# Kernel tuning notes

Hardware: AMD Instinct MI355X
Metric: run time of the kernel (lower is better)

The kernel has to match this reference:

```python
import jax, jax.numpy as jnp
import numpy as np

WIN = 8          # window_size
DIM = 96         # embedding dim
HEADS = 3        # num_heads
N = WIN * WIN    # tokens per window
B_ = 8192        # total windows (2 images * 64*64 windows)
NUM_WIN = 4096   # windows per image (mask leading dim)


def _relative_position_index():
    # Same construction as the torch module (meshgrid default 'ij').
    ch = np.arange(WIN)
    coords = np.stack(np.meshgrid(ch, ch, indexing="ij"))          # [2, W, W]
    flat = coords.reshape(2, -1)                                     # [2, N]
    rel = flat[:, :, None] - flat[:, None, :]                        # [2, N, N]
    rel = rel.transpose(1, 2, 0).astype(np.int32)                    # [N, N, 2]
    rel[:, :, 0] += WIN - 1
    rel[:, :, 1] += WIN - 1
    rel[:, :, 0] *= 2 * WIN - 1
    return rel.sum(-1)                                               # [N, N] int32


def setup_inputs() -> dict:
    key = jax.random.key(0)
    ks = jax.random.split(key, 8)
    x = jax.random.normal(ks[0], (B_, N, DIM), dtype=jnp.float32)
    mask = jax.random.normal(ks[1], (NUM_WIN, N, N), dtype=jnp.float32)
    s = 0.02
    qkv_w = jax.random.normal(ks[2], (3 * DIM, DIM), dtype=jnp.float32) * s
    qkv_b = jax.random.normal(ks[3], (3 * DIM,), dtype=jnp.float32) * s
    proj_w = jax.random.normal(ks[4], (DIM, DIM), dtype=jnp.float32) * s
    proj_b = jax.random.normal(ks[5], (DIM,), dtype=jnp.float32) * s
    n_bias = (2 * WIN - 1) * (2 * WIN - 1)  # 225
    bias_table = jax.random.normal(ks[6], (n_bias, HEADS), dtype=jnp.float32) * s
    rel_idx = jnp.asarray(_relative_position_index())  # [N, N] int32
    return {"x": x, "mask": mask, "qkv_w": qkv_w, "qkv_b": qkv_b,
            "proj_w": proj_w, "proj_b": proj_b, "bias_table": bias_table,
            "rel_idx": rel_idx}


def reference(x, mask, qkv_w, qkv_b, proj_w, proj_b, bias_table, rel_idx):
    Bw, n, C = x.shape
    hd = C // HEADS
    scale = hd ** (-0.5)
    qkv = (x @ qkv_w.T + qkv_b).reshape(Bw, n, 3, HEADS, hd)
    qkv = jnp.transpose(qkv, (2, 0, 3, 1, 4))
    q, k, v = qkv[0], qkv[1], qkv[2]
    attn = jnp.einsum("bhqd,bhkd->bhqk", q * scale, k)              # [Bw, H, n, n]
    # relative position bias gather: [n, n, H] -> [H, n, n]
    bias = bias_table[rel_idx.reshape(-1)].reshape(n, n, HEADS)
    attn = attn + jnp.transpose(bias, (2, 0, 1))[None]
    # shift mask: broadcast over (batch, heads)
    nw = mask.shape[0]
    attn = attn.reshape(Bw // nw, nw, HEADS, n, n) + mask[None, :, None]
    attn = attn.reshape(Bw, HEADS, n, n)
    attn = jax.nn.softmax(attn, axis=-1)
    out = jnp.einsum("bhqk,bhkd->bhqd", attn, v)                    # [Bw, H, n, hd]
    out = jnp.transpose(out, (0, 2, 1, 3)).reshape(Bw, n, C)
    return out @ proj_w.T + proj_b
```

## Files before the change

### kernel.cpp

```cpp
#include <hip/hip_runtime.h>

typedef __attribute__((ext_vector_type(8))) short short8v;
typedef __attribute__((ext_vector_type(4))) float f32x4;

#define INVLN2 1.4426950408889634f

__device__ __forceinline__ ushort f2bf(float f) {
  union { float f; unsigned int u; } c; c.f = f;
  return (ushort)((c.u + 0x7FFFu + ((c.u >> 16) & 1u)) >> 16);
}

__device__ __forceinline__ unsigned cvtpk(float a, float b) {
  unsigned r;
  asm("v_cvt_pk_bf16_f32 %0, %1, %2" : "=v"(r) : "v"(a), "v"(b));
  return r;
}

__device__ __forceinline__ float exp2w(float x) {
#if __has_builtin(__builtin_amdgcn_exp2f)
  return __builtin_amdgcn_exp2f(x);
#else
  return __expf(x * 0.6931471805599453f);
#endif
}

__device__ __forceinline__ short8v bits8(unsigned a, unsigned b, unsigned c, unsigned d) {
  union { unsigned u[4]; short8v s; } cv;
  cv.u[0] = a; cv.u[1] = b; cv.u[2] = c; cv.u[3] = d;
  return cv.s;
}

__global__ __launch_bounds__(256) void setup_k(
    const float* __restrict__ qkv_w, const float* __restrict__ proj_w,
    const float* __restrict__ bias_table, const int* __restrict__ rel_idx,
    const float* __restrict__ qkv_b,
    ushort* __restrict__ qkv_wb, ushort* __restrict__ proj_wb,
    float* __restrict__ bias_comb, float* __restrict__ qkv_bs) {
  const float qs = 0.17677669529663687f * INVLN2;
  int idx = blockIdx.x * 256 + threadIdx.x;
  if (idx < 27648) {
    qkv_wb[idx] = f2bf(qkv_w[idx] * (idx < 9216 ? qs : 1.0f));
  } else if (idx < 36864) {
    int i = idx - 27648;
    proj_wb[i] = f2bf(proj_w[i]);
  } else if (idx < 49152) {
    int i = idx - 36864;
    int h = i / 4096, rc = i % 4096;
    bias_comb[i] = bias_table[rel_idx[rc] * 3 + h] * INVLN2;
  } else if (idx < 49440) {
    int i = idx - 49152;
    qkv_bs[i] = qkv_b[i] * (i < 96 ? qs : 1.0f);
  }
}

__global__ __launch_bounds__(256, 2) void winattn(
    const float* __restrict__ x, const float* __restrict__ mask,
    const ushort* __restrict__ qkv_wb, const ushort* __restrict__ proj_wb,
    const float* __restrict__ bias_comb, const float* __restrict__ qkv_bs,
    const float* __restrict__ proj_b, float* __restrict__ out) {
  __shared__ ushort klds[2][64][104];
  __shared__ ushort vts[2][96][64];

  const int bb = blockIdx.x;
  const int t = threadIdx.x;
  const int w = t >> 6;
  const int lane = t & 63;
  const int l15 = lane & 15;
  const int g = lane >> 4;
  const int qrow = w * 16 + l15;

  const bool ghi = (g >= 2);
  const int srcA = l15 + 16 * ((g & 1) * 2);
  const int srcB = srcA + 16;

  float4 xr4[2][3][2];
  #pragma unroll
  for (int u = 0; u < 2; ++u) {
    const float* xr = x + ((size_t)(bb + u * 4096) * 64 + qrow) * 96 + g * 8;
    #pragma unroll
    for (int ks3 = 0; ks3 < 3; ++ks3) {
      xr4[u][ks3][0] = *reinterpret_cast<const float4*>(xr + ks3 * 32);
      xr4[u][ks3][1] = *reinterpret_cast<const float4*>(xr + ks3 * 32 + 4);
    }
  }
  const float* mrow = mask + (size_t)bb * 4096 + qrow * 64;
  float4 mk4[4];
  #pragma unroll
  for (int tj = 0; tj < 4; ++tj)
    mk4[tj] = *reinterpret_cast<const float4*>(mrow + tj * 16 + g * 4);

  short8v xa[2][3];
  #pragma unroll
  for (int u = 0; u < 2; ++u)
    #pragma unroll
    for (int ks3 = 0; ks3 < 3; ++ks3) {
      const float4 a0 = xr4[u][ks3][0], a1 = xr4[u][ks3][1];
      xa[u][ks3] = bits8(cvtpk(a0.x, a0.y), cvtpk(a0.z, a0.w),
                         cvtpk(a1.x, a1.y), cvtpk(a1.z, a1.w));
    }

  unsigned qpk[2][6][2];
  short8v bfA[3];
  float4 qbA = {0.f, 0.f, 0.f, 0.f}, qbB;
  float vbA = 0.f, vbB;
  {
    const ushort* wr = qkv_wb + l15 * 96 + g * 8;
    bfA[0] = *reinterpret_cast<const short8v*>(wr);
    bfA[1] = *reinterpret_cast<const short8v*>(wr + 32);
    bfA[2] = *reinterpret_cast<const short8v*>(wr + 64);
    qbA = *reinterpret_cast<const float4*>(qkv_bs + g * 4);
  }
  #pragma unroll
  for (int nt = 0; nt < 18; ++nt) {
    short8v bfB[3];
    if (nt < 17) {
      const ushort* wr = qkv_wb + ((nt + 1) * 16 + l15) * 96 + g * 8;
      bfB[0] = *reinterpret_cast<const short8v*>(wr);
      bfB[1] = *reinterpret_cast<const short8v*>(wr + 32);
      bfB[2] = *reinterpret_cast<const short8v*>(wr + 64);
      if (nt + 1 < 12) qbB = *reinterpret_cast<const float4*>(qkv_bs + (nt + 1) * 16 + g * 4);
      else             vbB = qkv_bs[(nt + 1) * 16 + l15];
    }
    if (nt < 6) {
      #pragma unroll
      for (int u = 0; u < 2; ++u) {
        f32x4 acc = {0.f, 0.f, 0.f, 0.f};
        #pragma unroll
        for (int ks3 = 0; ks3 < 3; ++ks3)
          acc = __builtin_amdgcn_mfma_f32_16x16x32_bf16(bfA[ks3], xa[u][ks3], acc, 0, 0, 0);
        qpk[u][nt][0] = cvtpk(acc[0] + qbA.x, acc[1] + qbA.y);
        qpk[u][nt][1] = cvtpk(acc[2] + qbA.z, acc[3] + qbA.w);
      }
    } else if (nt < 12) {
      #pragma unroll
      for (int u = 0; u < 2; ++u) {
        f32x4 acc = {0.f, 0.f, 0.f, 0.f};
        #pragma unroll
        for (int ks3 = 0; ks3 < 3; ++ks3)
          acc = __builtin_amdgcn_mfma_f32_16x16x32_bf16(bfA[ks3], xa[u][ks3], acc, 0, 0, 0);
        uint2 pk = make_uint2(cvtpk(acc[0] + qbA.x, acc[1] + qbA.y),
                              cvtpk(acc[2] + qbA.z, acc[3] + qbA.w));
        *reinterpret_cast<uint2*>(&klds[u][qrow][(nt - 6) * 16 + g * 4]) = pk;
      }
    } else {
      const int vc = nt * 16 + l15 - 192;
      const int tk = (w * 16 + g * 4) ^ ((vc & 7) << 3);
      #pragma unroll
      for (int u = 0; u < 2; ++u) {
        f32x4 acc = {0.f, 0.f, 0.f, 0.f};
        #pragma unroll
        for (int ks3 = 0; ks3 < 3; ++ks3)
          acc = __builtin_amdgcn_mfma_f32_16x16x32_bf16(xa[u][ks3], bfA[ks3], acc, 0, 0, 0);
        uint2 pk = make_uint2(cvtpk(acc[0] + vbA, acc[1] + vbA),
                              cvtpk(acc[2] + vbA, acc[3] + vbA));
        *reinterpret_cast<uint2*>(&vts[u][vc][tk]) = pk;
      }
    }
    if (nt < 17) {
      bfA[0] = bfB[0]; bfA[1] = bfB[1]; bfA[2] = bfB[2];
      qbA = qbB; vbA = vbB;
    }
  }

  short8v qf[2][3];
  #pragma unroll
  for (int u = 0; u < 2; ++u)
    #pragma unroll
    for (int h = 0; h < 3; ++h) {
      unsigned dm[4];
      #pragma unroll
      for (int m = 0; m < 4; ++m) {
        const int sl = (m < 2) ? srcA : srcB;
        unsigned lo = __shfl(qpk[u][2 * h + 0][m & 1], sl);
        unsigned hi = __shfl(qpk[u][2 * h + 1][m & 1], sl);
        dm[m] = ghi ? hi : lo;
      }
      qf[u][h] = bits8(dm[0], dm[1], dm[2], dm[3]);
    }

  const float* bcb0 = bias_comb + qrow * 64;
  float4 bc4[3][4];
  #pragma unroll
  for (int h = 0; h < 3; ++h)
    #pragma unroll
    for (int tj = 0; tj < 4; ++tj)
      bc4[h][tj] = *reinterpret_cast<const float4*>(bcb0 + h * 4096 + tj * 16 + g * 4);
  float bmk[3][4][4];
  #pragma unroll
  for (int h = 0; h < 3; ++h)
    #pragma unroll
    for (int tj = 0; tj < 4; ++tj) {
      bmk[h][tj][0] = bc4[h][tj].x + mk4[tj].x * INVLN2;
      bmk[h][tj][1] = bc4[h][tj].y + mk4[tj].y * INVLN2;
      bmk[h][tj][2] = bc4[h][tj].z + mk4[tj].z * INVLN2;
      bmk[h][tj][3] = bc4[h][tj].w + mk4[tj].w * INVLN2;
    }

  __syncthreads();

  short8v ofv[3][2];

  #pragma unroll
  for (int h = 0; h < 3; ++h) {
    f32x4 s[2][4];
    #pragma unroll
    for (int tj = 0; tj < 4; ++tj) {
      #pragma unroll
      for (int u = 0; u < 2; ++u) {
        short8v kf = *reinterpret_cast<const short8v*>(&klds[u][tj * 16 + l15][h * 32 + g * 8]);
        f32x4 z = {0.f, 0.f, 0.f, 0.f};
        s[u][tj] = __builtin_amdgcn_mfma_f32_16x16x32_bf16(kf, qf[u][h], z, 0, 0, 0);
      }
    }
    #pragma unroll
    for (int tj = 0; tj < 4; ++tj)
      #pragma unroll
      for (int u = 0; u < 2; ++u)
        #pragma unroll
        for (int r = 0; r < 4; ++r) s[u][tj][r] += bmk[h][tj][r];
    float inv[2];
    #pragma unroll
    for (int u = 0; u < 2; ++u) {
      #pragma unroll
      for (int tj = 0; tj < 4; ++tj)
        #pragma unroll
        for (int r = 0; r < 4; ++r) s[u][tj][r] = exp2w(s[u][tj][r]);
      float sm = ((s[u][0][0] + s[u][0][1]) + (s[u][0][2] + s[u][0][3]))
               + ((s[u][1][0] + s[u][1][1]) + (s[u][1][2] + s[u][1][3]))
               + ((s[u][2][0] + s[u][2][1]) + (s[u][2][2] + s[u][2][3]))
               + ((s[u][3][0] + s[u][3][1]) + (s[u][3][2] + s[u][3][3]));
      sm += __shfl_xor(sm, 16);
      sm += __shfl_xor(sm, 32);
      inv[u] = __builtin_amdgcn_rcpf(sm);
    }
    unsigned ppk[2][4][2];
    #pragma unroll
    for (int u = 0; u < 2; ++u)
      #pragma unroll
      for (int tj = 0; tj < 4; ++tj) {
        ppk[u][tj][0] = cvtpk(s[u][tj][0], s[u][tj][1]);
        ppk[u][tj][1] = cvtpk(s[u][tj][2], s[u][tj][3]);
      }
    short8v pfv[2][2];
    #pragma unroll
    for (int u = 0; u < 2; ++u)
      #pragma unroll
      for (int ks2 = 0; ks2 < 2; ++ks2) {
        unsigned dm[4];
        #pragma unroll
        for (int m = 0; m < 4; ++m) {
          const int sl = (m < 2) ? srcA : srcB;
          unsigned lo = __shfl(ppk[u][ks2 * 2 + 0][m & 1], sl);
          unsigned hi = __shfl(ppk[u][ks2 * 2 + 1][m & 1], sl);
          dm[m] = ghi ? hi : lo;
        }
        pfv[u][ks2] = bits8(dm[0], dm[1], dm[2], dm[3]);
      }
    f32x4 oacc[2][2];
    #pragma unroll
    for (int u = 0; u < 2; ++u)
      #pragma unroll
      for (int nt = 0; nt < 2; ++nt) {
        const int vc = h * 32 + nt * 16 + l15;
        f32x4 o = {0.f, 0.f, 0.f, 0.f};
        #pragma unroll
        for (int ks2 = 0; ks2 < 2; ++ks2) {
          const int tk = (ks2 * 32 + g * 8) ^ ((vc & 7) << 3);
          short8v vf = *reinterpret_cast<const short8v*>(&vts[u][vc][tk]);
          o = __builtin_amdgcn_mfma_f32_16x16x32_bf16(vf, pfv[u][ks2], o, 0, 0, 0);
        }
        oacc[u][nt] = o;
      }
    #pragma unroll
    for (int u = 0; u < 2; ++u) {
      unsigned opk[2][2];
      #pragma unroll
      for (int nt = 0; nt < 2; ++nt) {
        opk[nt][0] = cvtpk(oacc[u][nt][0] * inv[u], oacc[u][nt][1] * inv[u]);
        opk[nt][1] = cvtpk(oacc[u][nt][2] * inv[u], oacc[u][nt][3] * inv[u]);
      }
      unsigned dm[4];
      #pragma unroll
      for (int m = 0; m < 4; ++m) {
        const int sl = (m < 2) ? srcA : srcB;
        unsigned lo = __shfl(opk[0][m & 1], sl);
        unsigned hi = __shfl(opk[1][m & 1], sl);
        dm[m] = ghi ? hi : lo;
      }
      ofv[h][u] = bits8(dm[0], dm[1], dm[2], dm[3]);
    }
  }

  f32x4 pacc[2][6];
  #pragma unroll
  for (int u = 0; u < 2; ++u)
    #pragma unroll
    for (int nt2 = 0; nt2 < 6; ++nt2) pacc[u][nt2] = (f32x4){0.f, 0.f, 0.f, 0.f};
  #pragma unroll
  for (int h = 0; h < 3; ++h) {
    #pragma unroll
    for (int nt2 = 0; nt2 < 6; ++nt2) {
      short8v pfw = *reinterpret_cast<const short8v*>(proj_wb + (nt2 * 16 + l15) * 96 + h * 32 + g * 8);
      #pragma unroll
      for (int u = 0; u < 2; ++u)
        pacc[u][nt2] = __builtin_amdgcn_mfma_f32_16x16x32_bf16(ofv[h][u], pfw, pacc[u][nt2], 0, 0, 0);
    }
  }

  float pb[6];
  #pragma unroll
  for (int nt2 = 0; nt2 < 6; ++nt2) pb[nt2] = proj_b[nt2 * 16 + l15];
  #pragma unroll
  for (int u = 0; u < 2; ++u) {
    float* ob = out + (size_t)(bb + u * 4096) * 6144 + (w * 16 + g * 4) * 96 + l15;
    #pragma unroll
    for (int nt2 = 0; nt2 < 6; ++nt2)
      #pragma unroll
      for (int r = 0; r < 4; ++r)
        ob[r * 96 + nt2 * 16] = pacc[u][nt2][r] + pb[nt2];
  }
}

extern "C" void kernel_launch(void* const* d_in, const int* in_sizes, int n_in,
                              void* d_out, int out_size, void* d_ws, size_t ws_size,
                              hipStream_t stream) {
  const float* x          = (const float*)d_in[0];
  const float* mask       = (const float*)d_in[1];
  const float* qkv_w      = (const float*)d_in[2];
  const float* qkv_b      = (const float*)d_in[3];
  const float* proj_w     = (const float*)d_in[4];
  const float* proj_b     = (const float*)d_in[5];
  const float* bias_table = (const float*)d_in[6];
  const int*   rel_idx    = (const int*)d_in[7];

  char* ws = (char*)d_ws;
  ushort* qkv_wb    = (ushort*)ws;
  ushort* proj_wb   = (ushort*)(ws + 55296);
  float*  bias_comb = (float*)(ws + 55296 + 18432);
  float*  qkv_bs    = (float*)(ws + 55296 + 18432 + 49152);

  setup_k<<<194, 256, 0, stream>>>(qkv_w, proj_w, bias_table, rel_idx, qkv_b,
                                   qkv_wb, proj_wb, bias_comb, qkv_bs);
  winattn<<<4096, 256, 0, stream>>>(x, mask, qkv_wb, proj_wb,
                                    bias_comb, qkv_bs, proj_b, (float*)d_out);
}
```

Measured before the change: 167.5 us.

## Permute K, V^T and proj weight layouts to eliminate register shuffles between MFMAs

The reduction dimension of the K LDS tile, the V-transpose tile and the projection weights is permuted so that MFMA accumulator outputs can feed the next MFMA's operand directly. This removes the cross-lane __shfl sequences that previously rebuilt the Q, P and O fragments. The reduction order is the same permutation on both operands, so results stay mathematically equivalent, but correctness depends on the index maps matching exactly.

```diff
diff --git a/kernel.cpp b/kernel.cpp
--- a/kernel.cpp
+++ b/kernel.cpp
@@ -42,7 +42,11 @@
     qkv_wb[idx] = f2bf(qkv_w[idx] * (idx < 9216 ? qs : 1.0f));
   } else if (idx < 36864) {
     int i = idx - 27648;
-    proj_wb[i] = f2bf(proj_w[i]);
+    int cw = i / 96, j = i % 96;
+    int h = j >> 5, kk = j & 31;
+    int g = kk >> 3, b = (kk & 4) >> 2, d = kk & 3;
+    int src = h * 32 + 16 * b + 4 * g + d;
+    proj_wb[i] = f2bf(proj_w[cw * 96 + src]);
   } else if (idx < 49152) {
     int i = idx - 36864;
     int h = i / 4096, rc = i % 4096;
@@ -68,10 +72,6 @@
   const int l15 = lane & 15;
   const int g = lane >> 4;
   const int qrow = w * 16 + l15;
-
-  const bool ghi = (g >= 2);
-  const int srcA = l15 + 16 * ((g & 1) * 2);
-  const int srcB = srcA + 16;
 
   float4 xr4[2][3][2];
   #pragma unroll
@@ -132,6 +132,8 @@
         qpk[u][nt][1] = cvtpk(acc[2] + qbA.z, acc[3] + qbA.w);
       }
     } else if (nt < 12) {
+      const int m = nt - 6;
+      const int kcol = 32 * (m >> 1) + 8 * g + 4 * (m & 1);
       #pragma unroll
       for (int u = 0; u < 2; ++u) {
         f32x4 acc = {0.f, 0.f, 0.f, 0.f};
@@ -140,11 +142,11 @@
           acc = __builtin_amdgcn_mfma_f32_16x16x32_bf16(bfA[ks3], xa[u][ks3], acc, 0, 0, 0);
         uint2 pk = make_uint2(cvtpk(acc[0] + qbA.x, acc[1] + qbA.y),
                               cvtpk(acc[2] + qbA.z, acc[3] + qbA.w));
-        *reinterpret_cast<uint2*>(&klds[u][qrow][(nt - 6) * 16 + g * 4]) = pk;
+        *reinterpret_cast<uint2*>(&klds[u][qrow][kcol]) = pk;
       }
     } else {
       const int vc = nt * 16 + l15 - 192;
-      const int tk = (w * 16 + g * 4) ^ ((vc & 7) << 3);
+      const int tk = (32 * (w >> 1) + 8 * g + 4 * (w & 1)) ^ ((vc & 7) << 3);
       #pragma unroll
       for (int u = 0; u < 2; ++u) {
         f32x4 acc = {0.f, 0.f, 0.f, 0.f};
@@ -166,17 +168,9 @@
   #pragma unroll
   for (int u = 0; u < 2; ++u)
     #pragma unroll
-    for (int h = 0; h < 3; ++h) {
-      unsigned dm[4];
-      #pragma unroll
-      for (int m = 0; m < 4; ++m) {
-        const int sl = (m < 2) ? srcA : srcB;
-        unsigned lo = __shfl(qpk[u][2 * h + 0][m & 1], sl);
-        unsigned hi = __shfl(qpk[u][2 * h + 1][m & 1], sl);
-        dm[m] = ghi ? hi : lo;
-      }
-      qf[u][h] = bits8(dm[0], dm[1], dm[2], dm[3]);
-    }
+    for (int h = 0; h < 3; ++h)
+      qf[u][h] = bits8(qpk[u][2 * h][0], qpk[u][2 * h][1],
+                       qpk[u][2 * h + 1][0], qpk[u][2 * h + 1][1]);
 
   const float* bcb0 = bias_comb + qrow * 64;
   float4 bc4[3][4];
@@ -245,17 +239,9 @@
     #pragma unroll
     for (int u = 0; u < 2; ++u)
       #pragma unroll
-      for (int ks2 = 0; ks2 < 2; ++ks2) {
-        unsigned dm[4];
-        #pragma unroll
-        for (int m = 0; m < 4; ++m) {
-          const int sl = (m < 2) ? srcA : srcB;
-          unsigned lo = __shfl(ppk[u][ks2 * 2 + 0][m & 1], sl);
-          unsigned hi = __shfl(ppk[u][ks2 * 2 + 1][m & 1], sl);
-          dm[m] = ghi ? hi : lo;
-        }
-        pfv[u][ks2] = bits8(dm[0], dm[1], dm[2], dm[3]);
-      }
+      for (int ks2 = 0; ks2 < 2; ++ks2)
+        pfv[u][ks2] = bits8(ppk[u][2 * ks2][0], ppk[u][2 * ks2][1],
+                            ppk[u][2 * ks2 + 1][0], ppk[u][2 * ks2 + 1][1]);
     f32x4 oacc[2][2];
     #pragma unroll
     for (int u = 0; u < 2; ++u)
@@ -273,21 +259,11 @@
       }
     #pragma unroll
     for (int u = 0; u < 2; ++u) {
-      unsigned opk[2][2];
-      #pragma unroll
-      for (int nt = 0; nt < 2; ++nt) {
-        opk[nt][0] = cvtpk(oacc[u][nt][0] * inv[u], oacc[u][nt][1] * inv[u]);
-        opk[nt][1] = cvtpk(oacc[u][nt][2] * inv[u], oacc[u][nt][3] * inv[u]);
-      }
-      unsigned dm[4];
-      #pragma unroll
-      for (int m = 0; m < 4; ++m) {
-        const int sl = (m < 2) ? srcA : srcB;
-        unsigned lo = __shfl(opk[0][m & 1], sl);
-        unsigned hi = __shfl(opk[1][m & 1], sl);
-        dm[m] = ghi ? hi : lo;
-      }
-      ofv[h][u] = bits8(dm[0], dm[1], dm[2], dm[3]);
+      unsigned o00 = cvtpk(oacc[u][0][0] * inv[u], oacc[u][0][1] * inv[u]);
+      unsigned o01 = cvtpk(oacc[u][0][2] * inv[u], oacc[u][0][3] * inv[u]);
+      unsigned o10 = cvtpk(oacc[u][1][0] * inv[u], oacc[u][1][1] * inv[u]);
+      unsigned o11 = cvtpk(oacc[u][1][2] * inv[u], oacc[u][1][3] * inv[u]);
+      ofv[h][u] = bits8(o00, o01, o10, o11);
     }
   }
 
```

Result: no change. 165.1 us (-1.5%).
